# Performance work log

Measured on AMD Instinct MI355X. Metric: run time of the kernel, lower is better.

The kernel has to match this reference:

```python
import jax, jax.numpy as jnp
import numpy as np

B = 524288
H = 20          # heads
NUM_EX = 13     # embedding rows
EMB = 3         # embedding dim
FEAT_IN, FEAT_OUT = 3, 5
HEAD_IN, HEAD_HID = 8, 10


def setup_inputs() -> dict:
    key = jax.random.key(0)
    ks = jax.random.split(key, 12)
    e = jax.random.randint(ks[0], (B, H), 0, NUM_EX)
    f = jax.random.normal(ks[1], (B, H * FEAT_IN), dtype=jnp.float32)
    # embedding table; row 0 zeroed as in the torch __init__
    emb = jax.random.normal(ks[2], (NUM_EX, EMB), dtype=jnp.float32) * 0.1
    emb = emb.at[0].set(0.0)
    # features Linear(3 -> 5), stored as (in, out) so y = x @ Wf + bf
    Wf = jax.random.normal(ks[3], (FEAT_IN, FEAT_OUT), dtype=jnp.float32) * 0.5
    bf = jax.random.normal(ks[4], (FEAT_OUT,), dtype=jnp.float32) * 0.1
    # 20 parallel head MLPs, batched over the head axis
    W1 = jax.random.normal(ks[5], (H, HEAD_IN, HEAD_HID), dtype=jnp.float32) * 0.3
    b1 = jax.random.normal(ks[6], (H, HEAD_HID), dtype=jnp.float32) * 0.1
    W2 = jax.random.normal(ks[7], (H, HEAD_HID), dtype=jnp.float32) * 0.3
    b2 = jax.random.normal(ks[8], (H,), dtype=jnp.float32) * 0.1
    # output Linear(20 -> 1)
    Wo = jax.random.normal(ks[9], (H, 1), dtype=jnp.float32) * 0.3
    bo = jax.random.normal(ks[10], (1,), dtype=jnp.float32) * 0.1
    return {"e": e, "f": f, "emb": emb, "Wf": Wf, "bf": bf,
            "W1": W1, "b1": b1, "W2": W2, "b2": b2, "Wo": Wo, "bo": bo}


def reference(e, f, emb, Wf, bf, W1, b1, W2, b2, Wo, bo):
    ev = emb[e]                                    # (B, 20, 3) embedding lookup
    fv = f.reshape(-1, H, FEAT_IN) @ Wf + bf       # (B, 20, 5)
    x = jnp.concatenate([ev, fv], axis=2)          # (B, 20, 8)
    # all 20 heads as one batched matmul instead of a Python loop
    h1 = jax.nn.leaky_relu(jnp.einsum('bhi,hio->bho', x, W1) + b1)  # (B, 20, 10)
    h = jax.nn.softplus(jnp.einsum('bho,ho->bh', h1, W2) + b2)      # (B, 20)
    return h @ Wo + bo                             # (B, 1)
```

## Files before the change

kernel.cpp:

```cpp
#include <hip/hip_runtime.h>


#define HH   20
#define NEX  13
#define TST  12
#define WS_M 0
#define WS_T 640

__device__ __forceinline__ float softplus_fast(float x) {
    return fmaxf(x, 0.0f) + __logf(1.0f + __expf(-fabsf(x)));
}

__global__ void airfit_setup(const float* __restrict__ emb,
                             const float* __restrict__ Wf,
                             const float* __restrict__ bf,
                             const float* __restrict__ W1,
                             const float* __restrict__ b1,
                             float* __restrict__ ws)
{
    int t = blockIdx.x * 256 + threadIdx.x;
    if (t < HH * 3 * 10) {
        int h = t / 30, c = (t / 10) % 3, o = t % 10;
        float a = 0.0f;
        for (int q = 0; q < 5; ++q)
            a += Wf[c * 5 + q] * W1[(h * 8 + 3 + q) * 10 + o];
        ws[WS_M + (h * 3 + c) * 10 + o] = a;
    }
    if (t < HH * NEX * 10) {
        int h = t / (NEX * 10), idx = (t / 10) % NEX, o = t % 10;
        float a = b1[h * 10 + o];
        for (int i = 0; i < 3; ++i)
            a += emb[idx * 3 + i] * W1[(h * 8 + i) * 10 + o];
        for (int q = 0; q < 5; ++q)
            a += bf[q] * W1[(h * 8 + 3 + q) * 10 + o];
        ws[WS_T + (h * NEX + idx) * TST + o] = a;
    }
}

template<int J>
__device__ __forceinline__ float head_group(
    int4 iv, float4 fa, float4 fb, float4 fc,
    const float* __restrict__ s_T,
    const float* __restrict__ M,
    const float* __restrict__ W2, const float* __restrict__ b2,
    const float* __restrict__ Wo)
{
    int   ii[4]  = { iv.x, iv.y, iv.z, iv.w };
    float ff[12] = { fa.x, fa.y, fa.z, fa.w,
                     fb.x, fb.y, fb.z, fb.w,
                     fc.x, fc.y, fc.z, fc.w };
    float partial = 0.0f;

#pragma unroll
    for (int t = 0; t < 4; ++t) {
        const int h = 4 * J + t;
        const float* Trow = s_T + (h * NEX + ii[t]) * TST;
        float4 t0 = *reinterpret_cast<const float4*>(Trow);
        float4 t1 = *reinterpret_cast<const float4*>(Trow + 4);
        float2 t2 = *reinterpret_cast<const float2*>(Trow + 8);
        float pre[10] = { t0.x, t0.y, t0.z, t0.w,
                          t1.x, t1.y, t1.z, t1.w, t2.x, t2.y };

        float g0 = ff[3 * t + 0], g1 = ff[3 * t + 1], g2 = ff[3 * t + 2];
        float hacc = b2[h];
#pragma unroll
        for (int o = 0; o < 10; ++o) {
            float a = pre[o];
            a = fmaf(g0, M[(h * 3 + 0) * 10 + o], a);
            a = fmaf(g1, M[(h * 3 + 1) * 10 + o], a);
            a = fmaf(g2, M[(h * 3 + 2) * 10 + o], a);
            a = fmaxf(a, 0.01f * a);
            hacc = fmaf(a, W2[h * 10 + o], hacc);
        }
        partial = fmaf(softplus_fast(hacc), Wo[h], partial);
    }
    return partial;
}

__global__ __launch_bounds__(320, 6) void airfit_kernel(
    const int*   __restrict__ e,   const float* __restrict__ f,
    const float* __restrict__ ws,  const float* __restrict__ W2,
    const float* __restrict__ b2,  const float* __restrict__ Wo,
    const float* __restrict__ bo,  float* __restrict__ out, int B)
{
    __shared__ float s_T[HH * NEX * TST];
    __shared__ float s_part[5][64];

    for (int t = threadIdx.x; t < HH * NEX * TST; t += 320)
        s_T[t] = ws[WS_T + t];
    __syncthreads();

    const int i    = threadIdx.x & 63;
    const int jj   = threadIdx.x >> 6;
    const int item = blockIdx.x * 64 + i;
    const float* M = ws + WS_M;

    if (item < B) {
        int4 iv = *(reinterpret_cast<const int4*>(e + (size_t)item * HH) + jj);
        const float4* fp =
            reinterpret_cast<const float4*>(f + (size_t)item * (HH * 3)) + 3 * jj;
        float4 fa = fp[0], fb = fp[1], fc = fp[2];

        const int j = __builtin_amdgcn_readfirstlane(jj);
        float partial;
        switch (j) {
        case 0:  partial = head_group<0>(iv, fa, fb, fc, s_T, M, W2, b2, Wo); break;
        case 1:  partial = head_group<1>(iv, fa, fb, fc, s_T, M, W2, b2, Wo); break;
        case 2:  partial = head_group<2>(iv, fa, fb, fc, s_T, M, W2, b2, Wo); break;
        case 3:  partial = head_group<3>(iv, fa, fb, fc, s_T, M, W2, b2, Wo); break;
        default: partial = head_group<4>(iv, fa, fb, fc, s_T, M, W2, b2, Wo); break;
        }
        s_part[jj][i] = partial;
    }
    __syncthreads();

    if (jj == 0 && item < B) {
        float r = bo[0] + s_part[0][i] + s_part[1][i] + s_part[2][i]
                        + s_part[3][i] + s_part[4][i];
        out[item] = r;
    }
}

extern "C" void kernel_launch(void* const* d_in, const int* in_sizes, int n_in,
                              void* d_out, int out_size, void* d_ws, size_t ws_size,
                              hipStream_t stream) {
    const int*   e   = (const int*)  d_in[0];
    const float* f   = (const float*)d_in[1];
    const float* emb = (const float*)d_in[2];
    const float* Wf  = (const float*)d_in[3];
    const float* bf  = (const float*)d_in[4];
    const float* W1  = (const float*)d_in[5];
    const float* b1  = (const float*)d_in[6];
    const float* W2  = (const float*)d_in[7];
    const float* b2  = (const float*)d_in[8];
    const float* Wo  = (const float*)d_in[9];
    const float* bo  = (const float*)d_in[10];
    float* out = (float*)d_out;
    float* ws  = (float*)d_ws;

    int B = in_sizes[0] / HH;

    airfit_setup<<<11, 256, 0, stream>>>(emb, Wf, bf, W1, b1, ws);

    int blocks = (B + 63) / 64;
    airfit_kernel<<<blocks, 320, 0, stream>>>(e, f, ws, W2, b2, Wo, bo, out, B);
}
```

Baseline: 269.8 us.

## Compute all heads per thread, dropping cross-wave shared-memory reduction

Each thread now processes one batch item across all 20 heads instead of splitting heads across five wavefronts. This removes the shared-memory partial-sum buffer, the second block barrier and the per-wave switch dispatch. In exchange each thread carries a longer serial dependency chain and more registers, and its strided per-item loads are no longer spread over several wavefronts.

Result: slower. 286.0 us (+6.0%).

```diff
diff --git a/kernel.cpp b/kernel.cpp
--- a/kernel.cpp
+++ b/kernel.cpp
@@ -37,88 +37,64 @@
     }
 }
 
-template<int J>
-__device__ __forceinline__ float head_group(
-    int4 iv, float4 fa, float4 fb, float4 fc,
-    const float* __restrict__ s_T,
-    const float* __restrict__ M,
-    const float* __restrict__ W2, const float* __restrict__ b2,
-    const float* __restrict__ Wo)
-{
-    int   ii[4]  = { iv.x, iv.y, iv.z, iv.w };
-    float ff[12] = { fa.x, fa.y, fa.z, fa.w,
-                     fb.x, fb.y, fb.z, fb.w,
-                     fc.x, fc.y, fc.z, fc.w };
-    float partial = 0.0f;
-
-#pragma unroll
-    for (int t = 0; t < 4; ++t) {
-        const int h = 4 * J + t;
-        const float* Trow = s_T + (h * NEX + ii[t]) * TST;
-        float4 t0 = *reinterpret_cast<const float4*>(Trow);
-        float4 t1 = *reinterpret_cast<const float4*>(Trow + 4);
-        float2 t2 = *reinterpret_cast<const float2*>(Trow + 8);
-        float pre[10] = { t0.x, t0.y, t0.z, t0.w,
-                          t1.x, t1.y, t1.z, t1.w, t2.x, t2.y };
-
-        float g0 = ff[3 * t + 0], g1 = ff[3 * t + 1], g2 = ff[3 * t + 2];
-        float hacc = b2[h];
-#pragma unroll
-        for (int o = 0; o < 10; ++o) {
-            float a = pre[o];
-            a = fmaf(g0, M[(h * 3 + 0) * 10 + o], a);
-            a = fmaf(g1, M[(h * 3 + 1) * 10 + o], a);
-            a = fmaf(g2, M[(h * 3 + 2) * 10 + o], a);
-            a = fmaxf(a, 0.01f * a);
-            hacc = fmaf(a, W2[h * 10 + o], hacc);
-        }
-        partial = fmaf(softplus_fast(hacc), Wo[h], partial);
-    }
-    return partial;
-}
-
-__global__ __launch_bounds__(320, 6) void airfit_kernel(
+__global__ __launch_bounds__(256, 8) void airfit_kernel(
     const int*   __restrict__ e,   const float* __restrict__ f,
     const float* __restrict__ ws,  const float* __restrict__ W2,
     const float* __restrict__ b2,  const float* __restrict__ Wo,
     const float* __restrict__ bo,  float* __restrict__ out, int B)
 {
     __shared__ float s_T[HH * NEX * TST];
-    __shared__ float s_part[5][64];
 
-    for (int t = threadIdx.x; t < HH * NEX * TST; t += 320)
+    for (int t = threadIdx.x; t < HH * NEX * TST; t += 256)
         s_T[t] = ws[WS_T + t];
     __syncthreads();
 
-    const int i    = threadIdx.x & 63;
-    const int jj   = threadIdx.x >> 6;
-    const int item = blockIdx.x * 64 + i;
+    int item = blockIdx.x * 256 + threadIdx.x;
+    if (item >= B) return;
+
+    const int4*   ep = reinterpret_cast<const int4*>(e + (size_t)item * HH);
+    const float4* fp = reinterpret_cast<const float4*>(f + (size_t)item * (HH * 3));
     const float* M = ws + WS_M;
 
-    if (item < B) {
-        int4 iv = *(reinterpret_cast<const int4*>(e + (size_t)item * HH) + jj);
-        const float4* fp =
-            reinterpret_cast<const float4*>(f + (size_t)item * (HH * 3)) + 3 * jj;
-        float4 fa = fp[0], fb = fp[1], fc = fp[2];
+    float acc = bo[0];
 
-        const int j = __builtin_amdgcn_readfirstlane(jj);
-        float partial;
-        switch (j) {
-        case 0:  partial = head_group<0>(iv, fa, fb, fc, s_T, M, W2, b2, Wo); break;
-        case 1:  partial = head_group<1>(iv, fa, fb, fc, s_T, M, W2, b2, Wo); break;
-        case 2:  partial = head_group<2>(iv, fa, fb, fc, s_T, M, W2, b2, Wo); break;
-        case 3:  partial = head_group<3>(iv, fa, fb, fc, s_T, M, W2, b2, Wo); break;
-        default: partial = head_group<4>(iv, fa, fb, fc, s_T, M, W2, b2, Wo); break;
+#pragma unroll
+    for (int g = 0; g < 5; ++g) {
+        int4   iv = ep[g];
+        float4 fa = fp[3 * g + 0];
+        float4 fb = fp[3 * g + 1];
+        float4 fc = fp[3 * g + 2];
+        int   ii[4]  = { iv.x, iv.y, iv.z, iv.w };
+        float ff[12] = { fa.x, fa.y, fa.z, fa.w,
+                         fb.x, fb.y, fb.z, fb.w,
+                         fc.x, fc.y, fc.z, fc.w };
+
+#pragma unroll
+        for (int t = 0; t < 4; ++t) {
+            const int h = 4 * g + t;
+            const float* Trow = s_T + (h * NEX + ii[t]) * TST;
+            float4 t0 = *reinterpret_cast<const float4*>(Trow);
+            float4 t1 = *reinterpret_cast<const float4*>(Trow + 4);
+            float2 t2 = *reinterpret_cast<const float2*>(Trow + 8);
+            float pre[10] = { t0.x, t0.y, t0.z, t0.w,
+                              t1.x, t1.y, t1.z, t1.w, t2.x, t2.y };
+
+            float g0 = ff[3 * t + 0], g1 = ff[3 * t + 1], g2 = ff[3 * t + 2];
+            float hacc = b2[h];
+#pragma unroll
+            for (int o = 0; o < 10; ++o) {
+                float a = pre[o];
+                a = fmaf(g0, M[(h * 3 + 0) * 10 + o], a);
+                a = fmaf(g1, M[(h * 3 + 1) * 10 + o], a);
+                a = fmaf(g2, M[(h * 3 + 2) * 10 + o], a);
+                a = fmaxf(a, 0.01f * a);
+                hacc = fmaf(a, W2[h * 10 + o], hacc);
+            }
+            acc = fmaf(softplus_fast(hacc), Wo[h], acc);
         }
-        s_part[jj][i] = partial;
     }
-    __syncthreads();
 
-    if (jj == 0 && item < B) {
-        float r = bo[0] + s_part[0][i] + s_part[1][i] + s_part[2][i]
-                        + s_part[3][i] + s_part[4][i];
-        out[item] = r;
-    }
+    out[item] = acc;
 }
 
 extern "C" void kernel_launch(void* const* d_in, const int* in_sizes, int n_in,
@@ -142,6 +118,6 @@
 
     airfit_setup<<<11, 256, 0, stream>>>(emb, Wf, bf, W1, b1, ws);
 
-    int blocks = (B + 63) / 64;
-    airfit_kernel<<<blocks, 320, 0, stream>>>(e, f, ws, W2, b2, Wo, bo, out, B);
+    int blocks = (B + 255) / 256;
+    airfit_kernel<<<blocks, 256, 0, stream>>>(e, f, ws, W2, b2, Wo, bo, out, B);
 }
```
